# Kernel optimization log

Measured on AMD Instinct MI355X. Metric: run time of the kernel, lower is better.

## Reference

```python
import jax, jax.numpy as jnp
import numpy as np

N, K = 4096, 32          # batch, max active features per position
D = 49152                # half_feature_numel
BASE = 512               # base_dim
F0, F1 = 768, 64         # inter_dims of the two factored blocks


def setup_inputs() -> dict:
    key = jax.random.key(0)
    ks = jax.random.split(key, 8)
    return {
        "x_val": jnp.ones((N, K), dtype=jnp.float32),
        "W_aff": jax.random.normal(ks[0], (BASE, D), dtype=jnp.float32) * 0.01,
        "b_aff": jax.random.normal(ks[1], (BASE,), dtype=jnp.float32) * 0.01,
        "w_block0": jax.random.normal(ks[2], (F0, BASE), dtype=jnp.float32) * 0.01,
        "w_block1": jax.random.normal(ks[3], (F1, BASE), dtype=jnp.float32) * 0.01,
        "x_idx": jax.random.randint(ks[4], (N, K), 0, D, dtype=jnp.int32),
        "f0": jax.random.randint(ks[5], (D,), 0, F0, dtype=jnp.int32),
        "f1": jax.random.randint(ks[6], (D,), 0, F1, dtype=jnp.int32),
    }


def reference(x_val, W_aff, b_aff, w_block0, w_block1, x_idx, f0, f1):
    # affine(x): for sparse x, x_dense @ W_aff.T + b == sum_k v[n,k] * W_aff[:, idx[n,k]] + b
    aff_cols = W_aff.T[x_idx]                       # [N, K, BASE] gathered columns
    out = jnp.einsum('nk,nkd->nd', x_val, aff_cols) + b_aff
    # FactoredBlock: remap active indices through f, densify (duplicates sum), matmul.
    # Equivalent gather form: sum_k v[n,k] * weights[f[idx[n,k]]]
    out = out + jnp.einsum('nk,nkd->nd', x_val, w_block0[f0[x_idx]])
    out = out + jnp.einsum('nk,nkd->nd', x_val, w_block1[f1[x_idx]])
    return out
```

## Files before the change

### kernel.cpp

```cpp
#include <hip/hip_runtime.h>

#define N_BATCH 4096
#define K_ACT   32
#define D_FEAT  49152
#define BASE    512
#define F0_DIM  768
#define F1_DIM  64

__global__ __launch_bounds__(256) void build_R_kernel(
    const float* __restrict__ W_aff,
    const float* __restrict__ w0,
    const float* __restrict__ w1,
    const int* __restrict__ f0,
    const int* __restrict__ f1,
    float* __restrict__ R)
{
    __shared__ float tile[64 * 64];
    const int d0 = blockIdx.x * 64;
    const int r0 = blockIdx.y * 64;
    const int t  = threadIdx.x;
    const int q  = t >> 4;
    const int x  = t & 15;

    const float4* W4 = (const float4*)W_aff;
#pragma unroll
    for (int i = 0; i < 4; ++i) {
        const int rl = q + i * 16;
        float4 w = W4[(size_t)(r0 + rl) * (D_FEAT / 4) + (d0 >> 2) + x];
        const int sg = x ^ (rl >> 2);
        ((float4*)tile)[rl * 16 + sg] = w;
    }
    __syncthreads();

    const float4* w0v = (const float4*)w0;
    const float4* w1v = (const float4*)w1;
    float4*       R4  = (float4*)R;
#pragma unroll
    for (int i = 0; i < 4; ++i) {
        const int dl = q + i * 16;
        const int d  = d0 + dl;
        const int g  = dl >> 2;
        const int e  = dl & 3;
        float4 acc;
        float* accp = (float*)&acc;
#pragma unroll
        for (int j = 0; j < 4; ++j) {
            const int rl = 4 * x + j;
            accp[j] = tile[rl * 64 + ((g ^ x) << 2) + e];
        }
        const int i0 = f0[d];
        const int i1 = f1[d];
        const float4 a0 = w0v[(size_t)i0 * (BASE / 4) + (r0 >> 2) + x];
        const float4 a1 = w1v[(size_t)i1 * (BASE / 4) + (r0 >> 2) + x];
        acc.x += a0.x + a1.x;
        acc.y += a0.y + a1.y;
        acc.z += a0.z + a1.z;
        acc.w += a0.w + a1.w;
        R4[(size_t)d * (BASE / 4) + (r0 >> 2) + x] = acc;
    }
}

__global__ __launch_bounds__(256) void gather_out_kernel(
    const float* __restrict__ R,
    const float* __restrict__ x_val,
    const int*   __restrict__ x_idx,
    const float* __restrict__ b_aff,
    float* __restrict__ out)
{
    const int lane = threadIdx.x & 127;
    const int sub  = threadIdx.x >> 7;
    const int n    = blockIdx.x * 2 + sub;

    const float4* Rv = (const float4*)R;
    float4 acc = ((const float4*)b_aff)[lane];

    const int*   idxp = x_idx + (size_t)n * K_ACT;
    const float* valp = x_val + (size_t)n * K_ACT;

#pragma unroll
    for (int k = 0; k < K_ACT; ++k) {
        const int   idx = idxp[k];
        const float v   = valp[k];
        const float4 w = Rv[(size_t)idx * (BASE / 4) + lane];
        acc.x += v * w.x;
        acc.y += v * w.y;
        acc.z += v * w.z;
        acc.w += v * w.w;
    }
    ((float4*)out)[(size_t)n * (BASE / 4) + lane] = acc;
}

__global__ __launch_bounds__(512) void direct_kernel(
    const float* __restrict__ x_val,
    const float* __restrict__ W_aff,
    const float* __restrict__ b_aff,
    const float* __restrict__ w0,
    const float* __restrict__ w1,
    const int*   __restrict__ x_idx,
    const int*   __restrict__ f0,
    const int*   __restrict__ f1,
    float* __restrict__ out)
{
    const int n = blockIdx.x;
    const int r = threadIdx.x;
    float acc = b_aff[r];
    for (int k = 0; k < K_ACT; ++k) {
        const int   idx = x_idx[(size_t)n * K_ACT + k];
        const float v   = x_val[(size_t)n * K_ACT + k];
        float w = W_aff[(size_t)r * D_FEAT + idx];
        w += w0[(size_t)f0[idx] * BASE + r];
        w += w1[(size_t)f1[idx] * BASE + r];
        acc += v * w;
    }
    out[(size_t)n * BASE + r] = acc;
}

extern "C" void kernel_launch(void* const* d_in, const int* in_sizes, int n_in,
                              void* d_out, int out_size, void* d_ws, size_t ws_size,
                              hipStream_t stream) {
    const float* x_val = (const float*)d_in[0];
    const float* W_aff = (const float*)d_in[1];
    const float* b_aff = (const float*)d_in[2];
    const float* w0    = (const float*)d_in[3];
    const float* w1    = (const float*)d_in[4];
    const int*   x_idx = (const int*)d_in[5];
    const int*   f0    = (const int*)d_in[6];
    const int*   f1    = (const int*)d_in[7];
    float* out = (float*)d_out;

    const size_t needR = (size_t)D_FEAT * BASE * sizeof(float);
    if (ws_size >= needR) {
        float* R = (float*)d_ws;
        dim3 grid(D_FEAT / 64, BASE / 64);
        build_R_kernel<<<grid, 256, 0, stream>>>(W_aff, w0, w1, f0, f1, R);
        gather_out_kernel<<<N_BATCH / 2, 256, 0, stream>>>(R, x_val, x_idx, b_aff, out);
    } else {
        direct_kernel<<<N_BATCH, BASE, 0, stream>>>(x_val, W_aff, b_aff, w0, w1,
                                                    x_idx, f0, f1, out);
    }
}
```

Measured before the change: 218.0 us.

## Store combined weight table R in bf16 and gather bf16 rows

The intermediate table R (transposed W_aff plus the remapped factored block rows) is now written as bf16 with round-to-nearest-even instead of fp32. This halves the write traffic in the build kernel and the gather traffic in the output kernel, both of which are bandwidth bound. The build grid order is swapped so r-tiles vary fastest, which may improve locality. Threads are also remapped to 8 elements each, and each wavefront now handles one batch row. The cost is reduced precision in the summed weights, which may fail tight tolerances.

```diff
diff --git a/kernel.cpp b/kernel.cpp
--- a/kernel.cpp
+++ b/kernel.cpp
@@ -4,8 +4,15 @@
 #define K_ACT   32
 #define D_FEAT  49152
 #define BASE    512
-#define F0_DIM  768
-#define F1_DIM  64
+
+typedef unsigned short ushort_t;
+typedef __attribute__((ext_vector_type(8))) unsigned short ushort8;
+
+__device__ __forceinline__ ushort_t f2bf(float f) {
+    unsigned u = __builtin_bit_cast(unsigned, f);
+    u += 0x7FFFu + ((u >> 16) & 1u);
+    return (ushort_t)(u >> 16);
+}
 
 __global__ __launch_bounds__(256) void build_R_kernel(
     const float* __restrict__ W_aff,
@@ -13,66 +20,75 @@
     const float* __restrict__ w1,
     const int* __restrict__ f0,
     const int* __restrict__ f1,
-    float* __restrict__ R)
+    ushort_t* __restrict__ Rb)
 {
     __shared__ float tile[64 * 64];
-    const int d0 = blockIdx.x * 64;
-    const int r0 = blockIdx.y * 64;
+    const int r0 = blockIdx.x * 64;
+    const int d0 = blockIdx.y * 64;
     const int t  = threadIdx.x;
-    const int q  = t >> 4;
-    const int x  = t & 15;
 
-    const float4* W4 = (const float4*)W_aff;
+    {
+        const int q = t >> 4;
+        const int x = t & 15;
+        const float4* W4 = (const float4*)W_aff;
 #pragma unroll
-    for (int i = 0; i < 4; ++i) {
-        const int rl = q + i * 16;
-        float4 w = W4[(size_t)(r0 + rl) * (D_FEAT / 4) + (d0 >> 2) + x];
-        const int sg = x ^ (rl >> 2);
-        ((float4*)tile)[rl * 16 + sg] = w;
+        for (int i = 0; i < 4; ++i) {
+            const int rl = q + i * 16;
+            float4 w = W4[(size_t)(r0 + rl) * (D_FEAT / 4) + (d0 >> 2) + x];
+            ((float4*)tile)[rl * 16 + (x ^ (rl >> 2))] = w;
+        }
     }
     __syncthreads();
 
+    const int rg = t & 7;
+    const int dq = t >> 3;
     const float4* w0v = (const float4*)w0;
     const float4* w1v = (const float4*)w1;
-    float4*       R4  = (float4*)R;
 #pragma unroll
-    for (int i = 0; i < 4; ++i) {
-        const int dl = q + i * 16;
+    for (int i = 0; i < 2; ++i) {
+        const int dl = dq + 32 * i;
         const int d  = d0 + dl;
-        const int g  = dl >> 2;
-        const int e  = dl & 3;
-        float4 acc;
-        float* accp = (float*)&acc;
-#pragma unroll
-        for (int j = 0; j < 4; ++j) {
-            const int rl = 4 * x + j;
-            accp[j] = tile[rl * 64 + ((g ^ x) << 2) + e];
-        }
         const int i0 = f0[d];
         const int i1 = f1[d];
-        const float4 a0 = w0v[(size_t)i0 * (BASE / 4) + (r0 >> 2) + x];
-        const float4 a1 = w1v[(size_t)i1 * (BASE / 4) + (r0 >> 2) + x];
-        acc.x += a0.x + a1.x;
-        acc.y += a0.y + a1.y;
-        acc.z += a0.z + a1.z;
-        acc.w += a0.w + a1.w;
-        R4[(size_t)d * (BASE / 4) + (r0 >> 2) + x] = acc;
+        float a[8];
+#pragma unroll
+        for (int j = 0; j < 8; ++j) {
+            const int rl = 8 * rg + j;
+            a[j] = tile[rl * 64 + (((dl >> 2) ^ (rl >> 2)) << 2) + (dl & 3)];
+        }
+        const float4 b0 = w0v[(size_t)i0 * (BASE / 4) + (r0 >> 2) + 2 * rg];
+        const float4 b1 = w0v[(size_t)i0 * (BASE / 4) + (r0 >> 2) + 2 * rg + 1];
+        const float4 c0 = w1v[(size_t)i1 * (BASE / 4) + (r0 >> 2) + 2 * rg];
+        const float4 c1 = w1v[(size_t)i1 * (BASE / 4) + (r0 >> 2) + 2 * rg + 1];
+        a[0] += b0.x + c0.x;  a[1] += b0.y + c0.y;
+        a[2] += b0.z + c0.z;  a[3] += b0.w + c0.w;
+        a[4] += b1.x + c1.x;  a[5] += b1.y + c1.y;
+        a[6] += b1.z + c1.z;  a[7] += b1.w + c1.w;
+        ushort8 o;
+#pragma unroll
+        for (int j = 0; j < 8; ++j) o[j] = f2bf(a[j]);
+        *(ushort8*)&Rb[(size_t)d * BASE + r0 + 8 * rg] = o;
     }
 }
 
 __global__ __launch_bounds__(256) void gather_out_kernel(
-    const float* __restrict__ R,
+    const ushort_t* __restrict__ Rb,
     const float* __restrict__ x_val,
     const int*   __restrict__ x_idx,
     const float* __restrict__ b_aff,
     float* __restrict__ out)
 {
-    const int lane = threadIdx.x & 127;
-    const int sub  = threadIdx.x >> 7;
-    const int n    = blockIdx.x * 2 + sub;
+    const int lane = threadIdx.x & 63;
+    const int wv   = threadIdx.x >> 6;
+    const int n    = blockIdx.x * 4 + wv;
 
-    const float4* Rv = (const float4*)R;
-    float4 acc = ((const float4*)b_aff)[lane];
+    float acc[8];
+    {
+        const float4 bb0 = ((const float4*)b_aff)[2 * lane];
+        const float4 bb1 = ((const float4*)b_aff)[2 * lane + 1];
+        acc[0] = bb0.x; acc[1] = bb0.y; acc[2] = bb0.z; acc[3] = bb0.w;
+        acc[4] = bb1.x; acc[5] = bb1.y; acc[6] = bb1.z; acc[7] = bb1.w;
+    }
 
     const int*   idxp = x_idx + (size_t)n * K_ACT;
     const float* valp = x_val + (size_t)n * K_ACT;
@@ -81,13 +97,19 @@
     for (int k = 0; k < K_ACT; ++k) {
         const int   idx = idxp[k];
         const float v   = valp[k];
-        const float4 w = Rv[(size_t)idx * (BASE / 4) + lane];
-        acc.x += v * w.x;
-        acc.y += v * w.y;
-        acc.z += v * w.z;
-        acc.w += v * w.w;
+        const ushort8 w = *(const ushort8*)&Rb[(size_t)idx * BASE + 8 * lane];
+#pragma unroll
+        for (int j = 0; j < 8; ++j) {
+            const float wf = __builtin_bit_cast(float, (unsigned)w[j] << 16);
+            acc[j] = fmaf(v, wf, acc[j]);
+        }
     }
-    ((float4*)out)[(size_t)n * (BASE / 4) + lane] = acc;
+
+    float4 o0, o1;
+    o0.x = acc[0]; o0.y = acc[1]; o0.z = acc[2]; o0.w = acc[3];
+    o1.x = acc[4]; o1.y = acc[5]; o1.z = acc[6]; o1.w = acc[7];
+    ((float4*)out)[(size_t)n * (BASE / 4) + 2 * lane]     = o0;
+    ((float4*)out)[(size_t)n * (BASE / 4) + 2 * lane + 1] = o1;
 }
 
 __global__ __launch_bounds__(512) void direct_kernel(
@@ -128,12 +150,12 @@
     const int*   f1    = (const int*)d_in[7];
     float* out = (float*)d_out;
 
-    const size_t needR = (size_t)D_FEAT * BASE * sizeof(float);
+    const size_t needR = (size_t)D_FEAT * BASE * sizeof(ushort_t);
     if (ws_size >= needR) {
-        float* R = (float*)d_ws;
-        dim3 grid(D_FEAT / 64, BASE / 64);
-        build_R_kernel<<<grid, 256, 0, stream>>>(W_aff, w0, w1, f0, f1, R);
-        gather_out_kernel<<<N_BATCH / 2, 256, 0, stream>>>(R, x_val, x_idx, b_aff, out);
+        ushort_t* Rb = (ushort_t*)d_ws;
+        dim3 grid(BASE / 64, D_FEAT / 64);
+        build_R_kernel<<<grid, 256, 0, stream>>>(W_aff, w0, w1, f0, f1, Rb);
+        gather_out_kernel<<<N_BATCH / 4, 256, 0, stream>>>(Rb, x_val, x_idx, b_aff, out);
     } else {
         direct_kernel<<<N_BATCH, BASE, 0, stream>>>(x_val, W_aff, b_aff, w0, w1,
                                                     x_idx, f0, f1, out);
```

Measured after the change: 195.1 us. 1.12x faster.
